# Optimization experiments

Hardware: AMD Instinct MI355X
Metric: run time of the kernel (lower is better)

The kernel has to match this reference:

```python
import jax, jax.numpy as jnp
import numpy as np

NU, NM = 100000, 20000
E, EUU = 1000000, 500000
DU, DM, H = 64, 128, 128
BN_EPS = 1e-5


def _sage(x_src, x_dst, src, dst, Wl, bl, Wr):
    # PyG SAGEConv (mean aggr): lin_l(mean_j x_src[j]) + lin_r(x_dst)
    n_dst = x_dst.shape[0]
    msg = x_src[src]                                   # [E, H] gather
    agg = jax.ops.segment_sum(msg, dst, num_segments=n_dst)
    cnt = jax.ops.segment_sum(jnp.ones((dst.shape[0],), x_src.dtype), dst, num_segments=n_dst)
    agg = agg / jnp.maximum(cnt, 1.0)[:, None]
    return agg @ Wl + bl + x_dst @ Wr


def setup_inputs() -> dict:
    key = jax.random.key(0)
    ks = iter(jax.random.split(key, 40))
    s = 0.08  # weight scale for numerical stability
    d = {}
    d['user_feat'] = jax.random.normal(next(ks), (NU, DU), jnp.float32)
    d['movie_feat'] = jax.random.normal(next(ks), (NM, DM), jnp.float32)
    d['W_user'] = jax.random.normal(next(ks), (DU, H), jnp.float32) * s
    d['b_user'] = jnp.zeros((H,), jnp.float32)
    d['W_movie'] = jax.random.normal(next(ks), (DM, H), jnp.float32) * s
    d['b_movie'] = jnp.zeros((H,), jnp.float32)
    for name in ['u2m1', 'm2u1', 'u2m2', 'm2u2', 'u2u']:
        d[name + '_Wl'] = jax.random.normal(next(ks), (H, H), jnp.float32) * s
        d[name + '_bl'] = jnp.zeros((H,), jnp.float32)
        d[name + '_Wr'] = jax.random.normal(next(ks), (H, H), jnp.float32) * s
    d['p1_W'] = jax.random.normal(next(ks), (2 * H, H), jnp.float32) * s
    d['p1_b'] = jnp.zeros((H,), jnp.float32)
    d['bn_gamma'] = jnp.ones((H,), jnp.float32)
    d['bn_beta'] = jnp.zeros((H,), jnp.float32)
    d['bn_mean'] = jnp.zeros((H,), jnp.float32)
    d['bn_var'] = jax.random.uniform(next(ks), (H,), jnp.float32, 0.5, 1.5)
    d['p2_W'] = jax.random.normal(next(ks), (H, 1), jnp.float32) * s
    d['p2_b'] = jnp.zeros((1,), jnp.float32)
    d['rated_src'] = jax.random.randint(next(ks), (E,), 0, NU, jnp.int32)
    d['rated_dst'] = jax.random.randint(next(ks), (E,), 0, NM, jnp.int32)
    d['uu_src'] = jax.random.randint(next(ks), (EUU,), 0, NU, jnp.int32)
    d['uu_dst'] = jax.random.randint(next(ks), (EUU,), 0, NU, jnp.int32)
    return d


def reference(user_feat, movie_feat, W_user, b_user, W_movie, b_movie,
              u2m1_Wl, u2m1_bl, u2m1_Wr, m2u1_Wl, m2u1_bl, m2u1_Wr,
              u2m2_Wl, u2m2_bl, u2m2_Wr, m2u2_Wl, m2u2_bl, m2u2_Wr,
              u2u_Wl, u2u_bl, u2u_Wr,
              p1_W, p1_b, bn_gamma, bn_beta, bn_mean, bn_var, p2_W, p2_b,
              rated_src, rated_dst, uu_src, uu_dst):
    relu = jax.nn.relu
    ux = relu(user_feat @ W_user + b_user)     # [NU, H]
    mx = relu(movie_feat @ W_movie + b_movie)  # [NM, H]
    # user -> movie, movie -> user (reversed edges), twice
    mx = relu(_sage(ux, mx, rated_src, rated_dst, u2m1_Wl, u2m1_bl, u2m1_Wr))
    ux = relu(_sage(mx, ux, rated_dst, rated_src, m2u1_Wl, m2u1_bl, m2u1_Wr))
    mx = relu(_sage(ux, mx, rated_src, rated_dst, u2m2_Wl, u2m2_bl, u2m2_Wr))
    ux = relu(_sage(mx, ux, rated_dst, rated_src, m2u2_Wl, m2u2_bl, m2u2_Wr))
    # user -> user follows
    ux = relu(_sage(ux, ux, uu_src, uu_dst, u2u_Wl, u2u_bl, u2u_Wr))
    # edge embedding + MLP predictor (BN/Dropout in eval mode)
    emb = jnp.concatenate([ux[rated_src], mx[rated_dst]], axis=1)  # [E, 2H]
    h = emb @ p1_W + p1_b
    h = (h - bn_mean) * jax.lax.rsqrt(bn_var + BN_EPS) * bn_gamma + bn_beta
    h = relu(h)
    pred = jax.nn.sigmoid(h @ p2_W + p2_b)[:, 0]
    return pred * 4.0 + 1.0
```

## Files before the change

kernel.cpp:

```cpp
#include <hip/hip_runtime.h>
#include <cmath>


#define NUSR 100000
#define NMOV 20000
#define NEDG 1000000
#define NEUU 500000
#define DH 128

#define CAPM 96
#define CAPU 32
#define CAPUU 24

#define NBD 128
#define WD 157
#define NBS 128
#define WS 782
#define NBU 196
#define WU 512
#define NBT (NBD + NBS + NBU)

#define LCD 36
#define LCS 36
#define LCU 20
#define BKD 8448
#define BKS 8448
#define BKU 2944

#define NBINB 977
#define EPSL 32
#define NEPB (EPSL * 128)

#define GLU ((NUSR + 127) / 128)
#define GLM ((NMOV + 127) / 128)
#define GSU 512
#define GSM 157

typedef unsigned short ushort_t;
typedef unsigned char uchar_t;
typedef __attribute__((ext_vector_type(8))) short short8;
typedef __attribute__((ext_vector_type(4))) float f32x4;
typedef __attribute__((ext_vector_type(2))) float f32x2;

__device__ __forceinline__ ushort_t f2bf(float f) {
  unsigned u = __float_as_uint(f);
  u += 0x7FFFu + ((u >> 16) & 1u);
  return (ushort_t)(u >> 16);
}
__device__ __forceinline__ uchar_t f2fp8(float v) {
  return (uchar_t)(__builtin_amdgcn_cvt_pk_fp8_f32(v, v, 0, false) & 0xFF);
}
__device__ __forceinline__ void fp8x8_to_f32(uint2 v, float* f) {
  f32x2 a = __builtin_amdgcn_cvt_pk_f32_fp8((int)v.x, false);
  f32x2 b = __builtin_amdgcn_cvt_pk_f32_fp8((int)v.x, true);
  f32x2 c = __builtin_amdgcn_cvt_pk_f32_fp8((int)v.y, false);
  f32x2 d = __builtin_amdgcn_cvt_pk_f32_fp8((int)v.y, true);
  f[0] = a.x; f[1] = a.y; f[2] = b.x; f[3] = b.y;
  f[4] = c.x; f[5] = c.y; f[6] = d.x; f[7] = d.y;
}
__device__ __forceinline__ void bf2x8(int4 v, float* f) {
  unsigned a = (unsigned)v.x, b = (unsigned)v.y, c = (unsigned)v.z, d = (unsigned)v.w;
  f[0] = __uint_as_float(a << 16); f[1] = __uint_as_float(a & 0xFFFF0000u);
  f[2] = __uint_as_float(b << 16); f[3] = __uint_as_float(b & 0xFFFF0000u);
  f[4] = __uint_as_float(c << 16); f[5] = __uint_as_float(c & 0xFFFF0000u);
  f[6] = __uint_as_float(d << 16); f[7] = __uint_as_float(d & 0xFFFF0000u);
}
__device__ __forceinline__ int ntl(const int* p) { return __builtin_nontemporal_load(p); }
__device__ __forceinline__ unsigned ntl(const unsigned* p) { return __builtin_nontemporal_load(p); }
__device__ __forceinline__ ushort_t ntl(const ushort_t* p) { return __builtin_nontemporal_load(p); }

struct PrepArgs {
  const float* Wl[6];
  const float* Wr[6];
};
__global__ __launch_bounds__(256) void prep_all_k(
    PrepArgs pa, ushort_t* __restrict__ Wt,
    const float* __restrict__ W_user, const float* __restrict__ W_movie,
    ushort_t* __restrict__ WtU, ushort_t* __restrict__ WtM,
    const float* __restrict__ p1b, const float* __restrict__ gamma,
    const float* __restrict__ beta, const float* __restrict__ mean,
    const float* __restrict__ var,
    float* __restrict__ SEP, float* __restrict__ TEP,
    int* __restrict__ bcnt)
{
  int blk = blockIdx.x;
  if (blk < 768) {
    int wi = blk >> 7;
    int idx = (blk & 127) * 256 + threadIdx.x;
    int n = idx >> 8, k = idx & 255;
    const float* Wl = pa.Wl[wi];
    const float* Wr = pa.Wr[wi];
    float v = (k < DH) ? Wl[k * DH + n] : Wr[(k - DH) * DH + n];
    if (wi == 5) v *= gamma[n] * rsqrtf(var[n] + 1e-5f);
    Wt[(size_t)wi * 32768 + n * 256 + k] = f2bf(v);
  } else if (blk < 800) {
    int idx = (blk - 768) * 256 + threadIdx.x;
    int n = idx >> 6, k = idx & 63;
    WtU[n * 64 + k] = f2bf(W_user[k * DH + n]);
  } else if (blk < 864) {
    int idx = (blk - 800) * 256 + threadIdx.x;
    int n = idx >> 7, k = idx & 127;
    WtM[n * 128 + k] = f2bf(W_movie[k * DH + n]);
  } else {
    int f = threadIdx.x;
    if (f < DH) {
      float sc = gamma[f] * rsqrtf(var[f] + 1e-5f);
      SEP[f] = sc;
      TEP[f] = (p1b[f] - mean[f]) * sc + beta[f];
    }
    for (int i = threadIdx.x; i < NBT; i += 256) bcnt[i] = 0;
  }
}

__global__ __launch_bounds__(256) void bin_rated_k(
    const int* __restrict__ rsrc, const int* __restrict__ rdst,
    unsigned* __restrict__ bkt_d, uint2* __restrict__ bkt_s2,
    int* __restrict__ bcnt)
{
  __shared__ unsigned sb_d[NBD * LCD];
  __shared__ uint2 sb_s[NBS * LCS];
  __shared__ int lcnt[NBD + NBS];
  __shared__ int gbase[NBD + NBS];
  const int tid = threadIdx.x;
  for (int i = tid; i < NBD + NBS; i += 256) lcnt[i] = 0;
  __syncthreads();
  const int c = blockIdx.x;
#pragma unroll
  for (int it = 0; it < 4; ++it) {
    int e = c * 1024 + it * 256 + tid;
    if (e < NEDG) {
      int s = ntl(&rsrc[e]), d = ntl(&rdst[e]);
      int bd = d / WD;
      int o = atomicAdd(&lcnt[bd], 1);
      if (o < LCD) sb_d[bd * LCD + o] = (unsigned)(d - bd * WD) | ((unsigned)s << 8);
      int bs = s / WS;
      int o2 = atomicAdd(&lcnt[NBD + bs], 1);
      if (o2 < LCS)
        sb_s[bs * LCS + o2] =
            make_uint2((unsigned)(s - bs * WS) | ((unsigned)d << 10), (unsigned)e);
    }
  }
  __syncthreads();
  for (int i = tid; i < NBD + NBS; i += 256) {
    int n = lcnt[i];
    if (n > LCD) n = LCD;
    lcnt[i] = n;
    gbase[i] = atomicAdd(&bcnt[i], n);
  }
  __syncthreads();
  const int qw = tid >> 4, lq = tid & 15;
  for (int t = qw; t < NBD + NBS; t += 16) {
    int n = lcnt[t], gb = gbase[t];
    if (t < NBD) {
      if (gb + n > BKD) n = BKD - gb;
      unsigned* gp = bkt_d + (size_t)t * BKD;
      const unsigned* sp = sb_d + t * LCD;
      for (int i = lq; i < n; i += 16) gp[gb + i] = sp[i];
    } else {
      int b = t - NBD;
      if (gb + n > BKS) n = BKS - gb;
      uint2* gp = bkt_s2 + (size_t)b * BKS;
      const uint2* sp = sb_s + b * LCS;
      for (int i = lq; i < n; i += 16) gp[gb + i] = sp[i];
    }
  }
}

__global__ __launch_bounds__(256) void bin_uu_k(
    const int* __restrict__ usrc, const int* __restrict__ udst,
    unsigned* __restrict__ bkt_u, int* __restrict__ bcnt)
{
  __shared__ unsigned sb_u[NBU * LCU];
  __shared__ int lcnt[NBU];
  __shared__ int gbase[NBU];
  const int tid = threadIdx.x;
  for (int i = tid; i < NBU; i += 256) lcnt[i] = 0;
  __syncthreads();
  const int c = blockIdx.x;
#pragma unroll
  for (int it = 0; it < 2; ++it) {
    int e = c * 512 + it * 256 + tid;
    if (e < NEUU) {
      int s = ntl(&usrc[e]), d = ntl(&udst[e]);
      int bu = d >> 9;
      int o = atomicAdd(&lcnt[bu], 1);
      if (o < LCU) sb_u[bu * LCU + o] = (unsigned)(d & 511) | ((unsigned)s << 9);
    }
  }
  __syncthreads();
  for (int i = tid; i < NBU; i += 256) {
    int n = lcnt[i];
    if (n > LCU) n = LCU;
    lcnt[i] = n;
    gbase[i] = atomicAdd(&bcnt[NBD + NBS + i], n);
  }
  __syncthreads();
  const int qw = tid >> 4, lq = tid & 15;
  for (int t = qw; t < NBU; t += 16) {
    int n = lcnt[t], gb = gbase[t];
    if (gb + n > BKU) n = BKU - gb;
    unsigned* gp = bkt_u + (size_t)t * BKU;
    const unsigned* sp = sb_u + t * LCU;
    for (int i = lq; i < n; i += 16) gp[gb + i] = sp[i];
  }
}

__global__ __launch_bounds__(256) void csr_k(
    const unsigned* __restrict__ bkt_d, const uint2* __restrict__ bkt_s2,
    const unsigned* __restrict__ bkt_u, const int* __restrict__ bcnt,
    int* __restrict__ cnt_m, int* __restrict__ cnt_u, int* __restrict__ cnt_uu,
    int* __restrict__ col_m, ushort_t* __restrict__ col_u, int* __restrict__ col_uu)
{
  __shared__ int lc[WS];
  __shared__ alignas(16) unsigned cbuf[WD * CAPM];
  const int tid = threadIdx.x;
  const int bid = blockIdx.x;
  if (bid < NBD) {
    const int b = bid;
    const int nr = (NMOV - b * WD < WD) ? (NMOV - b * WD) : WD;
    for (int m = tid; m < nr; m += 256) lc[m] = 0;
    __syncthreads();
    int n = bcnt[b]; if (n > BKD) n = BKD;
    const unsigned* B = bkt_d + (size_t)b * BKD;
    for (int i = tid; i < n; i += 256) {
      unsigned v = ntl(&B[i]);
      int m = (int)(v & 255u);
      int o = atomicAdd(&lc[m], 1);
      if (o < CAPM) cbuf[m * CAPM + o] = v >> 8;
    }
    __syncthreads();
    for (int m = tid; m < nr; m += 256) cnt_m[b * WD + m] = lc[m];
    int4* dst = (int4*)(col_m + (size_t)b * WD * CAPM);
    const int4* src = (const int4*)cbuf;
    const int tot = nr * (CAPM / 4);
    for (int i = tid; i < tot; i += 256) dst[i] = src[i];
  } else if (bid < NBD + NBS) {
    const int b = bid - NBD;
    const int nr = (NUSR - b * WS < WS) ? (NUSR - b * WS) : WS;
    for (int u = tid; u < nr; u += 256) lc[u] = 0;
    __syncthreads();
    int n = bcnt[NBD + b]; if (n > BKS) n = BKS;
    const uint2* B = bkt_s2 + (size_t)b * BKS;
    ushort_t* cb16 = (ushort_t*)cbuf;
    for (int i = tid; i < n; i += 256) {
      unsigned v = B[i].x;
      int u = (int)(v & 1023u);
      int o = atomicAdd(&lc[u], 1);
      if (o < CAPU) cb16[u * CAPU + o] = (ushort_t)(v >> 10);
    }
    __syncthreads();
    for (int u = tid; u < nr; u += 256) cnt_u[b * WS + u] = lc[u];
    int4* dst = (int4*)(col_u + (size_t)b * WS * CAPU);
    const int4* src = (const int4*)cbuf;
    const int tot = nr * (CAPU / 8);
    for (int i = tid; i < tot; i += 256) dst[i] = src[i];
  } else {
    const int b = bid - NBD - NBS;
    const int nr = (NUSR - b * WU < WU) ? (NUSR - b * WU) : WU;
    for (int u = tid; u < nr; u += 256) lc[u] = 0;
    __syncthreads();
    int n = bcnt[NBD + NBS + b]; if (n > BKU) n = BKU;
    const unsigned* B = bkt_u + (size_t)b * BKU;
    for (int i = tid; i < n; i += 256) {
      unsigned v = ntl(&B[i]);
      int u = (int)(v & 511u);
      int o = atomicAdd(&lc[u], 1);
      if (o < CAPUU) cbuf[u * CAPUU + o] = v >> 9;
    }
    __syncthreads();
    for (int u = tid; u < nr; u += 256) cnt_uu[b * WU + u] = lc[u];
    int4* dst = (int4*)(col_uu + (size_t)b * WU * CAPUU);
    const int4* src = (const int4*)cbuf;
    const int tot = nr * (CAPUU / 4);
    for (int i = tid; i < tot; i += 256) dst[i] = src[i];
  }
}

template <int K>
__device__ __forceinline__ void lin_body(
    int lblk, const float* __restrict__ X, const ushort_t* __restrict__ Wt,
    const float* __restrict__ b, ushort_t* __restrict__ Y,
    uchar_t* __restrict__ Y8, int N)
{
  const int wave = threadIdx.x >> 6;
  const int lane = threadIdx.x & 63;
  const int row0 = (lblk * 4 + wave) * 32;
  if (row0 >= N) return;
  const int lm = lane & 15;
  const int koff = (lane >> 4) * 8;

  f32x4 acc[2][8];
#pragma unroll
  for (int a = 0; a < 2; ++a)
#pragma unroll
    for (int nt = 0; nt < 8; ++nt) acc[a][nt] = (f32x4){0.f, 0.f, 0.f, 0.f};

#pragma unroll
  for (int ks = 0; ks < K / 32; ++ks) {
    short8 af[2];
#pragma unroll
    for (int a = 0; a < 2; ++a) {
      const float* p = X + (size_t)(row0 + a * 16 + lm) * K + ks * 32 + koff;
      float4 v0 = *(const float4*)p;
      float4 v1 = *(const float4*)(p + 4);
      short8 s;
      s[0] = (short)f2bf(v0.x); s[1] = (short)f2bf(v0.y);
      s[2] = (short)f2bf(v0.z); s[3] = (short)f2bf(v0.w);
      s[4] = (short)f2bf(v1.x); s[5] = (short)f2bf(v1.y);
      s[6] = (short)f2bf(v1.z); s[7] = (short)f2bf(v1.w);
      af[a] = s;
    }
#pragma unroll
    for (int nt = 0; nt < 8; ++nt) {
      short8 bf = *(const short8*)&Wt[(nt * 16 + lm) * K + ks * 32 + koff];
      acc[0][nt] = __builtin_amdgcn_mfma_f32_16x16x32_bf16(af[0], bf, acc[0][nt], 0, 0, 0);
      acc[1][nt] = __builtin_amdgcn_mfma_f32_16x16x32_bf16(af[1], bf, acc[1][nt], 0, 0, 0);
    }
  }

  const int quad = lane >> 4;
  float bv[8];
#pragma unroll
  for (int nt = 0; nt < 8; ++nt) bv[nt] = b[nt * 16 + lm];
#pragma unroll
  for (int a = 0; a < 2; ++a) {
#pragma unroll
    for (int reg = 0; reg < 4; ++reg) {
      const int r = row0 + a * 16 + quad * 4 + reg;
      float vv[8];
#pragma unroll
      for (int nt = 0; nt < 8; ++nt)
        vv[nt] = fmaxf(acc[a][nt][reg] + bv[nt], 0.f);
#pragma unroll
      for (int nt = 0; nt < 8; ++nt)
        Y[(size_t)r * DH + nt * 16 + lm] = f2bf(vv[nt]);
#pragma unroll
      for (int nt = 0; nt < 8; ++nt)
        Y8[(size_t)r * DH + nt * 16 + lm] = f2fp8(vv[nt]);
    }
  }
}

__global__ __launch_bounds__(256) void lin2_k(
    const float* __restrict__ user_feat, const ushort_t* __restrict__ WtU,
    const float* __restrict__ b_user, ushort_t* __restrict__ ux, uchar_t* __restrict__ ux8,
    const float* __restrict__ movie_feat, const ushort_t* __restrict__ WtM,
    const float* __restrict__ b_movie, ushort_t* __restrict__ mx, uchar_t* __restrict__ mx8)
{
  const int blk = blockIdx.x;
  if (blk < GLU) lin_body<64>(blk, user_feat, WtU, b_user, ux, ux8, NUSR);
  else lin_body<128>(blk - GLU, movie_feat, WtM, b_movie, mx, mx8, NMOV);
}

template <typename CT, int CAP, int UNR>
__global__ __launch_bounds__(256) void agg_mean4_k(
    const uchar_t* __restrict__ x8, const int* __restrict__ cnt,
    const CT* __restrict__ col, ushort_t* __restrict__ out, int N)
{
  const int wave = threadIdx.x >> 6;
  const int lane = threadIdx.x & 63;
  const int lm = lane & 15, q = lane >> 4;
  const int row = blockIdx.x * 16 + wave * 4 + q;
  if (row >= N) return;
  const int deg = cnt[row];
  const int e = (deg < CAP) ? deg : CAP;
  const CT* crow = col + (size_t)row * CAP;
  float a[8];
#pragma unroll
  for (int j = 0; j < 8; ++j) a[j] = 0.f;
  int i = 0;
  if (UNR >= 16) {
    for (; i + 15 < e; i += 16) {
      uint2 v[16];
#pragma unroll
      for (int u = 0; u < 16; ++u) {
        int s = (int)ntl(&crow[i + u]);
        v[u] = *(const uint2*)(x8 + (size_t)s * DH + lm * 8);
      }
#pragma unroll
      for (int u = 0; u < 16; ++u) {
        float f0[8];
        fp8x8_to_f32(v[u], f0);
#pragma unroll
        for (int j = 0; j < 8; ++j) a[j] += f0[j];
      }
    }
  }
  if (UNR >= 8) {
    for (; i + 7 < e; i += 8) {
      uint2 v[8];
#pragma unroll
      for (int u = 0; u < 8; ++u) {
        int s = (int)ntl(&crow[i + u]);
        v[u] = *(const uint2*)(x8 + (size_t)s * DH + lm * 8);
      }
#pragma unroll
      for (int u = 0; u < 8; ++u) {
        float f0[8];
        fp8x8_to_f32(v[u], f0);
#pragma unroll
        for (int j = 0; j < 8; ++j) a[j] += f0[j];
      }
    }
  }
  for (; i + 3 < e; i += 4) {
    uint2 v0, v1, v2, v3;
    int s0 = (int)ntl(&crow[i]), s1 = (int)ntl(&crow[i + 1]);
    int s2 = (int)ntl(&crow[i + 2]), s3 = (int)ntl(&crow[i + 3]);
    v0 = *(const uint2*)(x8 + (size_t)s0 * DH + lm * 8);
    v1 = *(const uint2*)(x8 + (size_t)s1 * DH + lm * 8);
    v2 = *(const uint2*)(x8 + (size_t)s2 * DH + lm * 8);
    v3 = *(const uint2*)(x8 + (size_t)s3 * DH + lm * 8);
    float f0[8], f1[8], f2[8], f3[8];
    fp8x8_to_f32(v0, f0); fp8x8_to_f32(v1, f1);
    fp8x8_to_f32(v2, f2); fp8x8_to_f32(v3, f3);
#pragma unroll
    for (int j = 0; j < 8; ++j) a[j] += (f0[j] + f1[j]) + (f2[j] + f3[j]);
  }
  for (; i < e; ++i) {
    uint2 v0 = *(const uint2*)(x8 + (size_t)(int)ntl(&crow[i]) * DH + lm * 8);
    float f0[8];
    fp8x8_to_f32(v0, f0);
#pragma unroll
    for (int j = 0; j < 8; ++j) a[j] += f0[j];
  }
  float inv = 1.f / (float)(deg > 1 ? deg : 1);
  unsigned p0 = f2bf(a[0] * inv) | ((unsigned)f2bf(a[1] * inv) << 16);
  unsigned p1 = f2bf(a[2] * inv) | ((unsigned)f2bf(a[3] * inv) << 16);
  unsigned p2 = f2bf(a[4] * inv) | ((unsigned)f2bf(a[5] * inv) << 16);
  unsigned p3 = f2bf(a[6] * inv) | ((unsigned)f2bf(a[7] * inv) << 16);
  *(int4*)(out + (size_t)row * DH + lm * 8) = make_int4(p0, p1, p2, p3);
}

__global__ __launch_bounds__(256) void sage_mfma_k(
    const ushort_t* __restrict__ A0, const ushort_t* __restrict__ A1,
    const ushort_t* __restrict__ Wt, const float* __restrict__ bl,
    ushort_t* __restrict__ out, uchar_t* __restrict__ out8, int N)
{
  __shared__ alignas(16) ushort_t WtS[32768];
  const int tid = threadIdx.x;
  for (int f = tid; f < 4096; f += 256) {
    const int r = f >> 5, c = f & 31;
    const int4 v = *(const int4*)(Wt + (size_t)f * 8);
    *(int4*)&WtS[(size_t)((r << 5) | (c ^ (r & 31))) << 3] = v;
  }
  __syncthreads();

  const int wave = tid >> 6;
  const int lane = tid & 63;
  const int lm = lane & 15;
  const int kq = lane >> 4;
  const int koff = kq * 8;
  const int quad = kq;

  float bv[8];
#pragma unroll
  for (int nt = 0; nt < 8; ++nt) bv[nt] = bl[nt * 16 + lm];

  const int T = (N + 31) >> 5;
  for (int t = (int)blockIdx.x * 4 + wave; t < T; t += (int)gridDim.x * 4) {
    const int row0 = t * 32;
    size_t abase[2];
#pragma unroll
    for (int a = 0; a < 2; ++a) abase[a] = (size_t)(row0 + a * 16 + lm) * DH;

    f32x4 acc[2][8];
#pragma unroll
    for (int a = 0; a < 2; ++a)
#pragma unroll
      for (int nt = 0; nt < 8; ++nt) acc[a][nt] = (f32x4){0.f, 0.f, 0.f, 0.f};

#pragma unroll
    for (int ks = 0; ks < 8; ++ks) {
      short8 af[2];
#pragma unroll
      for (int a = 0; a < 2; ++a) {
        const ushort_t* p = (ks < 4) ? (A0 + abase[a] + ks * 32 + koff)
                                     : (A1 + abase[a] + (ks - 4) * 32 + koff);
        af[a] = *(const short8*)p;
      }
#pragma unroll
      for (int nt = 0; nt < 8; ++nt) {
        const int r = nt * 16 + lm;
        const int c = (ks * 4 + kq) ^ (r & 31);
        short8 bf = *(const short8*)&WtS[(size_t)((r << 5) | c) << 3];
        acc[0][nt] = __builtin_amdgcn_mfma_f32_16x16x32_bf16(af[0], bf, acc[0][nt], 0, 0, 0);
        acc[1][nt] = __builtin_amdgcn_mfma_f32_16x16x32_bf16(af[1], bf, acc[1][nt], 0, 0, 0);
      }
    }

#pragma unroll
    for (int a = 0; a < 2; ++a) {
#pragma unroll
      for (int reg = 0; reg < 4; ++reg) {
        const int r = row0 + a * 16 + quad * 4 + reg;
        float vv[8];
#pragma unroll
        for (int nt = 0; nt < 8; ++nt)
          vv[nt] = fmaxf(acc[a][nt][reg] + bv[nt], 0.f);
#pragma unroll
        for (int nt = 0; nt < 8; ++nt)
          out[(size_t)r * DH + nt * 16 + lm] = f2bf(vv[nt]);
        if (out8) {
#pragma unroll
          for (int nt = 0; nt < 8; ++nt)
            out8[(size_t)r * DH + nt * 16 + lm] = f2fp8(vv[nt]);
        }
      }
    }
  }
}

__device__ __forceinline__ void proj_body(
    int lblk, const ushort_t* __restrict__ A, const ushort_t* __restrict__ Wt,
    int kofs, const float* __restrict__ bias, ushort_t* __restrict__ out, int N)
{
  const int wave = threadIdx.x >> 6;
  const int lane = threadIdx.x & 63;
  const int row0 = (lblk * 4 + wave) * 32;
  if (row0 >= N) return;
  const int lm = lane & 15;
  const int koff = (lane >> 4) * 8;

  size_t abase[2];
#pragma unroll
  for (int a = 0; a < 2; ++a) abase[a] = (size_t)(row0 + a * 16 + lm) * DH;

  f32x4 acc[2][8];
#pragma unroll
  for (int a = 0; a < 2; ++a)
#pragma unroll
    for (int nt = 0; nt < 8; ++nt) acc[a][nt] = (f32x4){0.f, 0.f, 0.f, 0.f};

#pragma unroll
  for (int ks = 0; ks < 4; ++ks) {
    short8 af[2];
#pragma unroll
    for (int a = 0; a < 2; ++a) af[a] = *(const short8*)(A + abase[a] + ks * 32 + koff);
#pragma unroll
    for (int nt = 0; nt < 8; ++nt) {
      short8 bf = *(const short8*)&Wt[(nt * 16 + lm) * 256 + kofs + ks * 32 + koff];
      acc[0][nt] = __builtin_amdgcn_mfma_f32_16x16x32_bf16(af[0], bf, acc[0][nt], 0, 0, 0);
      acc[1][nt] = __builtin_amdgcn_mfma_f32_16x16x32_bf16(af[1], bf, acc[1][nt], 0, 0, 0);
    }
  }

  float bb[8];
#pragma unroll
  for (int nt = 0; nt < 8; ++nt) bb[nt] = bias ? bias[nt * 16 + lm] : 0.f;

  const int quad = lane >> 4;
#pragma unroll
  for (int a = 0; a < 2; ++a) {
#pragma unroll
    for (int reg = 0; reg < 4; ++reg) {
      const int r = row0 + a * 16 + quad * 4 + reg;
#pragma unroll
      for (int nt = 0; nt < 8; ++nt)
        out[(size_t)r * DH + nt * 16 + lm] = f2bf(acc[a][nt][reg] + bb[nt]);
    }
  }
}

__global__ __launch_bounds__(256) void proj2_k(
    const ushort_t* __restrict__ ux, const ushort_t* __restrict__ mx,
    const ushort_t* __restrict__ Wt, const float* __restrict__ TEP,
    ushort_t* __restrict__ pu, ushort_t* __restrict__ pm, int gmU)
{
  if ((int)blockIdx.x < gmU) proj_body(blockIdx.x, ux, Wt, 0, nullptr, pu, NUSR);
  else proj_body(blockIdx.x - gmU, mx, Wt, DH, TEP, pm, NMOV);
}

__global__ __launch_bounds__(256) void ep_bkt_k(
    const ushort_t* __restrict__ pu, const ushort_t* __restrict__ pm,
    const uint2* __restrict__ bkt_s2, const int* __restrict__ bcnt,
    const float* __restrict__ p2W, const float* __restrict__ p2b,
    float* __restrict__ out)
{
  const int b = (int)blockIdx.x & 127;
  const int sl = (int)blockIdx.x >> 7;
  const int tid = threadIdx.x;
  const int lm = tid & 15;
  const int qw = tid >> 4;
  const int f0 = lm * 8;

  float w2[8];
#pragma unroll
  for (int j = 0; j < 8; ++j) w2[j] = p2W[f0 + j];
  const float bias2 = p2b[0];

  int n = bcnt[NBD + b];
  if (n > BKS) n = BKS;
  const uint2* B = bkt_s2 + (size_t)b * BKS;
  const int ub = b * WS;
  const int chunk = (n + EPSL - 1) / EPSL;
  const int st = sl * chunk;
  int en = st + chunk;
  if (en > n) en = n;

  for (int i0 = st + qw; i0 < en; i0 += 64) {
    bool vld[4];
    uint2 ent[4];
    int4 uv[4], mv[4];
#pragma unroll
    for (int u = 0; u < 4; ++u) {
      const int ii = i0 + u * 16;
      vld[u] = (ii < en);
      ent[u] = B[vld[u] ? ii : i0];
    }
#pragma unroll
    for (int u = 0; u < 4; ++u) {
      const int s = ub + (int)(ent[u].x & 1023u);
      const int d = (int)(ent[u].x >> 10);
      uv[u] = *(const int4*)(pu + (s << 7) + f0);
      mv[u] = *(const int4*)(pm + (d << 7) + f0);
    }
#pragma unroll
    for (int u = 0; u < 4; ++u) {
      float fu[8], fm[8];
      bf2x8(uv[u], fu);
      bf2x8(mv[u], fm);
      float p = 0.f;
#pragma unroll
      for (int j = 0; j < 8; ++j) {
        float h = fmaxf(fu[j] + fm[j], 0.f);
        p = fmaf(h, w2[j], p);
      }
      p += __shfl_xor(p, 1, 16);
      p += __shfl_xor(p, 2, 16);
      p += __shfl_xor(p, 4, 16);
      p += __shfl_xor(p, 8, 16);
      if (lm == 0 && vld[u])
        __builtin_nontemporal_store(4.f / (1.f + expf(-(p + bias2))) + 1.f, &out[ent[u].y]);
    }
  }
}

extern "C" void kernel_launch(void* const* d_in, const int* in_sizes, int n_in,
                              void* d_out, int out_size, void* d_ws, size_t ws_size,
                              hipStream_t stream)
{
  const float* user_feat = (const float*)d_in[0];
  const float* movie_feat = (const float*)d_in[1];
  const float* W_user = (const float*)d_in[2];
  const float* b_user = (const float*)d_in[3];
  const float* W_movie = (const float*)d_in[4];
  const float* b_movie = (const float*)d_in[5];
  const float* u2m1_Wl = (const float*)d_in[6];
  const float* u2m1_bl = (const float*)d_in[7];
  const float* u2m1_Wr = (const float*)d_in[8];
  const float* m2u1_Wl = (const float*)d_in[9];
  const float* m2u1_bl = (const float*)d_in[10];
  const float* m2u1_Wr = (const float*)d_in[11];
  const float* u2m2_Wl = (const float*)d_in[12];
  const float* u2m2_bl = (const float*)d_in[13];
  const float* u2m2_Wr = (const float*)d_in[14];
  const float* m2u2_Wl = (const float*)d_in[15];
  const float* m2u2_bl = (const float*)d_in[16];
  const float* m2u2_Wr = (const float*)d_in[17];
  const float* u2u_Wl = (const float*)d_in[18];
  const float* u2u_bl = (const float*)d_in[19];
  const float* u2u_Wr = (const float*)d_in[20];
  const float* p1_W = (const float*)d_in[21];
  const float* p1_b = (const float*)d_in[22];
  const float* bn_gamma = (const float*)d_in[23];
  const float* bn_beta = (const float*)d_in[24];
  const float* bn_mean = (const float*)d_in[25];
  const float* bn_var = (const float*)d_in[26];
  const float* p2_W = (const float*)d_in[27];
  const float* p2_b = (const float*)d_in[28];
  const int* rated_src = (const int*)d_in[29];
  const int* rated_dst = (const int*)d_in[30];
  const int* uu_src = (const int*)d_in[31];
  const int* uu_dst = (const int*)d_in[32];

  ushort_t* ux = (ushort_t*)d_ws;
  ushort_t* mx = ux + (size_t)NUSR * DH;
  ushort_t* agg = mx + (size_t)NMOV * DH;
  ushort_t* pm = agg + (size_t)NUSR * DH;
  ushort_t* Wt = pm + (size_t)NMOV * DH;
  ushort_t* WtU = Wt + 6 * 32768;
  ushort_t* WtM = WtU + 8192;
  float* SEP = (float*)(WtM + 16384);
  float* TEP = SEP + DH;
  int* col_m = (int*)(TEP + DH);
  ushort_t* col_u = (ushort_t*)(col_m + (size_t)NMOV * CAPM);
  int* col_uu = (int*)(col_u + (size_t)NUSR * CAPU);
  int* cntbuf = col_uu + (size_t)NUSR * CAPUU;
  uchar_t* ux8 = (uchar_t*)(cntbuf + (NMOV + 2 * NUSR + NBT));
  uchar_t* mx8 = ux8 + (size_t)NUSR * DH;
  uint2* bkt_s2 = (uint2*)(mx8 + (size_t)NMOV * DH);
  int* cnt_m = cntbuf;
  int* cnt_u = cntbuf + NMOV;
  int* cnt_uu = cntbuf + NMOV + NUSR;
  int* bcnt = cntbuf + NMOV + 2 * NUSR;

  unsigned* bkt_d = (unsigned*)agg;
  unsigned* bkt_u = bkt_d + (size_t)NBD * BKD;

  ushort_t* Wt_u2m1 = Wt + 0 * 32768;
  ushort_t* Wt_m2u1 = Wt + 1 * 32768;
  ushort_t* Wt_u2m2 = Wt + 2 * 32768;
  ushort_t* Wt_m2u2 = Wt + 3 * 32768;
  ushort_t* Wt_u2u  = Wt + 4 * 32768;
  ushort_t* Wt_p1   = Wt + 5 * 32768;
  ushort_t* pu = agg;

  PrepArgs pa;
  pa.Wl[0] = u2m1_Wl; pa.Wr[0] = u2m1_Wr;
  pa.Wl[1] = m2u1_Wl; pa.Wr[1] = m2u1_Wr;
  pa.Wl[2] = u2m2_Wl; pa.Wr[2] = u2m2_Wr;
  pa.Wl[3] = m2u2_Wl; pa.Wr[3] = m2u2_Wr;
  pa.Wl[4] = u2u_Wl;  pa.Wr[4] = u2u_Wr;
  pa.Wl[5] = p1_W;    pa.Wr[5] = p1_W + DH * DH;
  prep_all_k<<<865, 256, 0, stream>>>(
      pa, Wt, W_user, W_movie, WtU, WtM,
      p1_b, bn_gamma, bn_beta, bn_mean, bn_var, SEP, TEP, bcnt);

  bin_rated_k<<<NBINB, 256, 0, stream>>>(
      rated_src, rated_dst, bkt_d, bkt_s2, bcnt);
  bin_uu_k<<<NBINB, 256, 0, stream>>>(uu_src, uu_dst, bkt_u, bcnt);
  csr_k<<<NBT, 256, 0, stream>>>(
      bkt_d, bkt_s2, bkt_u, bcnt, cnt_m, cnt_u, cnt_uu, col_m, col_u, col_uu);
  lin2_k<<<GLU + GLM, 256, 0, stream>>>(
      user_feat, WtU, b_user, ux, ux8, movie_feat, WtM, b_movie, mx, mx8);

  const int gaM = (NMOV + 15) / 16, gaU = (NUSR + 15) / 16;
  agg_mean4_k<int, CAPM, 16><<<gaM, 256, 0, stream>>>(ux8, cnt_m, col_m, agg, NMOV);
  sage_mfma_k<<<GSM, 256, 0, stream>>>(agg, mx, Wt_u2m1, u2m1_bl, mx, mx8, NMOV);
  agg_mean4_k<ushort_t, CAPU, 8><<<gaU, 256, 0, stream>>>(mx8, cnt_u, col_u, agg, NUSR);
  sage_mfma_k<<<GSU, 256, 0, stream>>>(agg, ux, Wt_m2u1, m2u1_bl, ux, ux8, NUSR);
  agg_mean4_k<int, CAPM, 16><<<gaM, 256, 0, stream>>>(ux8, cnt_m, col_m, agg, NMOV);
  sage_mfma_k<<<GSM, 256, 0, stream>>>(agg, mx, Wt_u2m2, u2m2_bl, mx, mx8, NMOV);
  agg_mean4_k<ushort_t, CAPU, 8><<<gaU, 256, 0, stream>>>(mx8, cnt_u, col_u, agg, NUSR);
  sage_mfma_k<<<GSU, 256, 0, stream>>>(agg, ux, Wt_m2u2, m2u2_bl, ux, ux8, NUSR);
  agg_mean4_k<int, CAPUU, 8><<<gaU, 256, 0, stream>>>(ux8, cnt_uu, col_uu, agg, NUSR);
  sage_mfma_k<<<GSU, 256, 0, stream>>>(agg, ux, Wt_u2u, u2u_bl, ux, (uchar_t*)nullptr, NUSR);

  const int gmU = (NUSR + 127) / 128, gmM = (NMOV + 127) / 128;
  proj2_k<<<gmU + gmM, 256, 0, stream>>>(ux, mx, Wt_p1, TEP, pu, pm, gmU);
  ep_bkt_k<<<NEPB, 256, 0, stream>>>(
      pu, pm, bkt_s2, bcnt, p2_W, p2_b, (float*)d_out);
}
```

Baseline: 551.9 us.

## Store bucket indices in user CSR and iterate edge predictor per user

The user-side CSR now stores each edge's position within its bucket instead of the movie id, so the movie→user aggregation takes an extra indirection through the bucket array to recover the source. The edge predictor kernel walks edges grouped by user via this CSR, loading each user's projected row once and reusing it across that user's edges instead of reloading it per edge. The cost is a dependent extra load per gathered neighbor in two aggregation passes, plus serialized per-user loops with uneven degree in the predictor. Edges beyond the CSR capacity per user would be skipped in the output.

```diff
diff --git a/kernel.cpp b/kernel.cpp
--- a/kernel.cpp
+++ b/kernel.cpp
@@ -246,7 +246,7 @@
       unsigned v = B[i].x;
       int u = (int)(v & 1023u);
       int o = atomicAdd(&lc[u], 1);
-      if (o < CAPU) cb16[u * CAPU + o] = (ushort_t)(v >> 10);
+      if (o < CAPU) cb16[u * CAPU + o] = (ushort_t)i;
     }
     __syncthreads();
     for (int u = tid; u < nr; u += 256) cnt_u[b * WS + u] = lc[u];
@@ -352,10 +352,11 @@
   else lin_body<128>(blk - GLU, movie_feat, WtM, b_movie, mx, mx8, NMOV);
 }
 
-template <typename CT, int CAP, int UNR>
+template <typename CT, int CAP, int UNR, bool IND>
 __global__ __launch_bounds__(256) void agg_mean4_k(
     const uchar_t* __restrict__ x8, const int* __restrict__ cnt,
-    const CT* __restrict__ col, ushort_t* __restrict__ out, int N)
+    const CT* __restrict__ col, const uint2* __restrict__ bkt,
+    ushort_t* __restrict__ out, int N)
 {
   const int wave = threadIdx.x >> 6;
   const int lane = threadIdx.x & 63;
@@ -365,18 +366,25 @@
   const int deg = cnt[row];
   const int e = (deg < CAP) ? deg : CAP;
   const CT* crow = col + (size_t)row * CAP;
+  const unsigned* Bb = nullptr;
+  if (IND) Bb = (const unsigned*)(bkt + (size_t)(row / WS) * BKS);
   float a[8];
 #pragma unroll
   for (int j = 0; j < 8; ++j) a[j] = 0.f;
   int i = 0;
   if (UNR >= 16) {
     for (; i + 15 < e; i += 16) {
+      int sx[16];
+#pragma unroll
+      for (int u = 0; u < 16; ++u) sx[u] = (int)ntl(&crow[i + u]);
+      if (IND) {
+#pragma unroll
+        for (int u = 0; u < 16; ++u) sx[u] = (int)(ntl(&Bb[sx[u] * 2]) >> 10);
+      }
       uint2 v[16];
 #pragma unroll
-      for (int u = 0; u < 16; ++u) {
-        int s = (int)ntl(&crow[i + u]);
-        v[u] = *(const uint2*)(x8 + (size_t)s * DH + lm * 8);
-      }
+      for (int u = 0; u < 16; ++u)
+        v[u] = *(const uint2*)(x8 + (size_t)sx[u] * DH + lm * 8);
 #pragma unroll
       for (int u = 0; u < 16; ++u) {
         float f0[8];
@@ -388,12 +396,17 @@
   }
   if (UNR >= 8) {
     for (; i + 7 < e; i += 8) {
+      int sx[8];
+#pragma unroll
+      for (int u = 0; u < 8; ++u) sx[u] = (int)ntl(&crow[i + u]);
+      if (IND) {
+#pragma unroll
+        for (int u = 0; u < 8; ++u) sx[u] = (int)(ntl(&Bb[sx[u] * 2]) >> 10);
+      }
       uint2 v[8];
 #pragma unroll
-      for (int u = 0; u < 8; ++u) {
-        int s = (int)ntl(&crow[i + u]);
-        v[u] = *(const uint2*)(x8 + (size_t)s * DH + lm * 8);
-      }
+      for (int u = 0; u < 8; ++u)
+        v[u] = *(const uint2*)(x8 + (size_t)sx[u] * DH + lm * 8);
 #pragma unroll
       for (int u = 0; u < 8; ++u) {
         float f0[8];
@@ -404,21 +417,27 @@
     }
   }
   for (; i + 3 < e; i += 4) {
-    uint2 v0, v1, v2, v3;
-    int s0 = (int)ntl(&crow[i]), s1 = (int)ntl(&crow[i + 1]);
-    int s2 = (int)ntl(&crow[i + 2]), s3 = (int)ntl(&crow[i + 3]);
-    v0 = *(const uint2*)(x8 + (size_t)s0 * DH + lm * 8);
-    v1 = *(const uint2*)(x8 + (size_t)s1 * DH + lm * 8);
-    v2 = *(const uint2*)(x8 + (size_t)s2 * DH + lm * 8);
-    v3 = *(const uint2*)(x8 + (size_t)s3 * DH + lm * 8);
+    int sx[4];
+#pragma unroll
+    for (int u = 0; u < 4; ++u) sx[u] = (int)ntl(&crow[i + u]);
+    if (IND) {
+#pragma unroll
+      for (int u = 0; u < 4; ++u) sx[u] = (int)(ntl(&Bb[sx[u] * 2]) >> 10);
+    }
+    uint2 v[4];
+#pragma unroll
+    for (int u = 0; u < 4; ++u)
+      v[u] = *(const uint2*)(x8 + (size_t)sx[u] * DH + lm * 8);
     float f0[8], f1[8], f2[8], f3[8];
-    fp8x8_to_f32(v0, f0); fp8x8_to_f32(v1, f1);
-    fp8x8_to_f32(v2, f2); fp8x8_to_f32(v3, f3);
+    fp8x8_to_f32(v[0], f0); fp8x8_to_f32(v[1], f1);
+    fp8x8_to_f32(v[2], f2); fp8x8_to_f32(v[3], f3);
 #pragma unroll
     for (int j = 0; j < 8; ++j) a[j] += (f0[j] + f1[j]) + (f2[j] + f3[j]);
   }
   for (; i < e; ++i) {
-    uint2 v0 = *(const uint2*)(x8 + (size_t)(int)ntl(&crow[i]) * DH + lm * 8);
+    int sx = (int)ntl(&crow[i]);
+    if (IND) sx = (int)(ntl(&Bb[sx * 2]) >> 10);
+    uint2 v0 = *(const uint2*)(x8 + (size_t)sx * DH + lm * 8);
     float f0[8];
     fp8x8_to_f32(v0, f0);
 #pragma unroll
@@ -573,7 +592,8 @@
 
 __global__ __launch_bounds__(256) void ep_bkt_k(
     const ushort_t* __restrict__ pu, const ushort_t* __restrict__ pm,
-    const uint2* __restrict__ bkt_s2, const int* __restrict__ bcnt,
+    const uint2* __restrict__ bkt_s2, const int* __restrict__ cnt_u,
+    const ushort_t* __restrict__ col_u,
     const float* __restrict__ p2W, const float* __restrict__ p2b,
     float* __restrict__ out)
 {
@@ -589,37 +609,27 @@
   for (int j = 0; j < 8; ++j) w2[j] = p2W[f0 + j];
   const float bias2 = p2b[0];
 
-  int n = bcnt[NBD + b];
-  if (n > BKS) n = BKS;
-  const uint2* B = bkt_s2 + (size_t)b * BKS;
-  const int ub = b * WS;
-  const int chunk = (n + EPSL - 1) / EPSL;
-  const int st = sl * chunk;
-  int en = st + chunk;
-  if (en > n) en = n;
-
-  for (int i0 = st + qw; i0 < en; i0 += 64) {
-    bool vld[4];
-    uint2 ent[4];
-    int4 uv[4], mv[4];
-#pragma unroll
-    for (int u = 0; u < 4; ++u) {
-      const int ii = i0 + u * 16;
-      vld[u] = (ii < en);
-      ent[u] = B[vld[u] ? ii : i0];
-    }
-#pragma unroll
-    for (int u = 0; u < 4; ++u) {
-      const int s = ub + (int)(ent[u].x & 1023u);
-      const int d = (int)(ent[u].x >> 10);
-      uv[u] = *(const int4*)(pu + (s << 7) + f0);
-      mv[u] = *(const int4*)(pm + (d << 7) + f0);
-    }
-#pragma unroll
-    for (int u = 0; u < 4; ++u) {
-      float fu[8], fm[8];
-      bf2x8(uv[u], fu);
-      bf2x8(mv[u], fm);
+  const uint2* B2 = bkt_s2 + (size_t)b * BKS;
+  const int u0 = b * WS;
+  const int nr = (NUSR - u0 < WS) ? (NUSR - u0) : WS;
+
+  for (int ul = sl * 16 + qw; ul < nr; ul += EPSL * 16) {
+    const int u = u0 + ul;
+    const int deg = cnt_u[u];
+    const int e = (deg < CAPU) ? deg : CAPU;
+    if (e <= 0) continue;
+    int4 uv = *(const int4*)(pu + ((size_t)u << 7) + f0);
+    float fu[8];
+    bf2x8(uv, fu);
+    const ushort_t* crow = col_u + (size_t)u * CAPU;
+    uint2 ent = B2[(int)crow[0]];
+    for (int o = 0; o < e; ++o) {
+      uint2 entn = ent;
+      if (o + 1 < e) entn = B2[(int)crow[o + 1]];
+      const int d = (int)(ent.x >> 10);
+      int4 mv = *(const int4*)(pm + ((size_t)d << 7) + f0);
+      float fm[8];
+      bf2x8(mv, fm);
       float p = 0.f;
 #pragma unroll
       for (int j = 0; j < 8; ++j) {
@@ -630,8 +640,9 @@
       p += __shfl_xor(p, 2, 16);
       p += __shfl_xor(p, 4, 16);
       p += __shfl_xor(p, 8, 16);
-      if (lm == 0 && vld[u])
-        __builtin_nontemporal_store(4.f / (1.f + expf(-(p + bias2))) + 1.f, &out[ent[u].y]);
+      if (lm == 0)
+        __builtin_nontemporal_store(4.f / (1.f + expf(-(p + bias2))) + 1.f, &out[ent.y]);
+      ent = entn;
     }
   }
 }
@@ -726,19 +737,24 @@
       user_feat, WtU, b_user, ux, ux8, movie_feat, WtM, b_movie, mx, mx8);
 
   const int gaM = (NMOV + 15) / 16, gaU = (NUSR + 15) / 16;
-  agg_mean4_k<int, CAPM, 16><<<gaM, 256, 0, stream>>>(ux8, cnt_m, col_m, agg, NMOV);
+  agg_mean4_k<int, CAPM, 16, false><<<gaM, 256, 0, stream>>>(
+      ux8, cnt_m, col_m, nullptr, agg, NMOV);
   sage_mfma_k<<<GSM, 256, 0, stream>>>(agg, mx, Wt_u2m1, u2m1_bl, mx, mx8, NMOV);
-  agg_mean4_k<ushort_t, CAPU, 8><<<gaU, 256, 0, stream>>>(mx8, cnt_u, col_u, agg, NUSR);
+  agg_mean4_k<ushort_t, CAPU, 8, true><<<gaU, 256, 0, stream>>>(
+      mx8, cnt_u, col_u, bkt_s2, agg, NUSR);
   sage_mfma_k<<<GSU, 256, 0, stream>>>(agg, ux, Wt_m2u1, m2u1_bl, ux, ux8, NUSR);
-  agg_mean4_k<int, CAPM, 16><<<gaM, 256, 0, stream>>>(ux8, cnt_m, col_m, agg, NMOV);
+  agg_mean4_k<int, CAPM, 16, false><<<gaM, 256, 0, stream>>>(
+      ux8, cnt_m, col_m, nullptr, agg, NMOV);
   sage_mfma_k<<<GSM, 256, 0, stream>>>(agg, mx, Wt_u2m2, u2m2_bl, mx, mx8, NMOV);
-  agg_mean4_k<ushort_t, CAPU, 8><<<gaU, 256, 0, stream>>>(mx8, cnt_u, col_u, agg, NUSR);
+  agg_mean4_k<ushort_t, CAPU, 8, true><<<gaU, 256, 0, stream>>>(
+      mx8, cnt_u, col_u, bkt_s2, agg, NUSR);
   sage_mfma_k<<<GSU, 256, 0, stream>>>(agg, ux, Wt_m2u2, m2u2_bl, ux, ux8, NUSR);
-  agg_mean4_k<int, CAPUU, 8><<<gaU, 256, 0, stream>>>(ux8, cnt_uu, col_uu, agg, NUSR);
+  agg_mean4_k<int, CAPUU, 8, false><<<gaU, 256, 0, stream>>>(
+      ux8, cnt_uu, col_uu, nullptr, agg, NUSR);
   sage_mfma_k<<<GSU, 256, 0, stream>>>(agg, ux, Wt_u2u, u2u_bl, ux, (uchar_t*)nullptr, NUSR);
 
   const int gmU = (NUSR + 127) / 128, gmM = (NMOV + 127) / 128;
   proj2_k<<<gmU + gmM, 256, 0, stream>>>(ux, mx, Wt_p1, TEP, pu, pm, gmU);
   ep_bkt_k<<<NEPB, 256, 0, stream>>>(
-      pu, pm, bkt_s2, bcnt, p2_W, p2_b, (float*)d_out);
-}
+      pu, pm, bkt_s2, cnt_u, col_u, p2_W, p2_b, (float*)d_out);
+}
```

New measurement: 613.1 us. +11.1%, slower.
